# Kernel optimization log

Hardware: AMD Instinct MI355X
Metric: run time of the kernel (lower is better)

## Reference

```python
import jax, jax.numpy as jnp
import numpy as np

B, L, C = 4, 2048, 1024
NH, HD, INTER, K = 16, 64, 256, 16
LR = 1.0
EPS = 1e-6

def gelu_tanh(x):
    return 0.5 * x * (1.0 + jnp.tanh(0.79788456 * (x + 0.044715 * x * x * x)))

def diff_gelu(x):
    t = jnp.tanh(0.79788456 * x * (1.0 + 0.044715 * x * x))
    return 0.5 * x * ((1.0 - t * t) * (0.79788456 + 0.1070322243 * x * x)) + 0.5 * (1.0 + t)

def setup_inputs():
    key = jax.random.key(0)
    ks = jax.random.split(key, 8)
    num_layers = 24
    return {
        'hidden_states': jax.random.normal(ks[0], (B, L, C), jnp.float32),
        'Wq': 0.02 * jax.random.normal(ks[1], (C, C), jnp.float32),
        'Wk': 0.02 * jax.random.normal(ks[2], (C, C), jnp.float32),
        'Wv': 0.02 * jax.random.normal(ks[3], (C, C), jnp.float32),
        'Wo': 0.02 * jax.random.normal(ks[4], (C, C), jnp.float32),
        'W1': 0.02 * jax.random.normal(ks[5], (NH, HD, INTER), jnp.float32),
        'b1': jnp.zeros((NH, 1, INTER), jnp.float32),
        'W2': (0.02 / np.sqrt(2 * num_layers)) * jax.random.normal(ks[6], (NH, INTER, HD), jnp.float32),
        'b2': jnp.zeros((NH, 1, HD), jnp.float32),
        'ln_weight': jnp.ones((NH, HD), jnp.float32),
        'ln_bias': jnp.zeros((NH, HD), jnp.float32),
        'gate_weight': 0.02 * jax.random.normal(ks[7], (NH, 1, C), jnp.float32),
        'gate_bias': jnp.zeros((NH, 1), jnp.float32),
    }

def _ln(z, w, b):
    mu = z.mean(-1, keepdims=True)
    var = z.var(-1, keepdims=True)
    return w * ((z - mu) * jax.lax.rsqrt(var + EPS)) + b

def _compute_chunk(carry, inp, ln_w, ln_b):
    # One inner-SGD chunk (dual form), per batch/head.
    W1, b1, W2, b2 = carry                       # [HD,INTER],[1,INTER],[INTER,HD],[1,HD]
    XA, XB, XC, coeff = inp                      # [K,HD],[K,HD],[K,HD],[K,1]
    Z1 = XB @ W1 + b1                            # [K,INTER]
    X2 = gelu_tanh(Z1)
    Z2 = X2 @ W2 + b2                            # [K,HD]
    DLN_out, ln_vjp = jax.vjp(lambda z: _ln(z, ln_w, ln_b), Z2)
    grad_Z2 = ln_vjp(DLN_out - XA)[0]            # d(recon loss)/dZ2
    grad_Z1 = (grad_Z2 @ W2.T) * diff_gelu(Z1)
    Attn1 = jnp.tril(XC @ XB.T)                  # [K,K] causal dual-form attention
    b1_bar = b1 - coeff * jnp.cumsum(grad_Z1, axis=0)
    Z1_bar = XC @ W1 - (coeff * Attn1) @ grad_Z1 + b1_bar
    X2_bar = gelu_tanh(Z1_bar)
    Attn2 = jnp.tril(X2_bar @ X2.T)
    b2_bar = b2 - coeff * jnp.cumsum(grad_Z2, axis=0)
    Z2_bar = X2_bar @ W2 - (coeff * Attn2) @ grad_Z2 + b2_bar
    W1n = W1 - (coeff[-1] * XB).T @ grad_Z1
    W2n = W2 - (coeff[-1] * X2).T @ grad_Z2
    return (W1n, b1_bar[-1:], W2n, b2_bar[-1:]), Z2_bar

def _per_head(XA, XB, XC, coeff, W1, b1, W2, b2, ln_w, ln_b):
    step = lambda c, i: _compute_chunk(c, i, ln_w, ln_b)
    _, ys = jax.lax.scan(step, (W1, b1, W2, b2), (XA, XB, XC, coeff))
    return ys                                    # [n_chunk,K,HD]

def reference(hidden_states, Wq, Wk, Wv, Wo, W1, b1, W2, b2, ln_weight, ln_bias, gate_weight, gate_bias):
    n_chunk = L // K
    X = hidden_states.reshape(B, n_chunk, K, C)
    def proj(W):
        return (hidden_states @ W.T).reshape(B, n_chunk, K, NH, HD).transpose(0, 3, 1, 2, 4)
    XA, XB, XC = proj(Wq), proj(Wk), proj(Wv)    # [B,NH,n_chunk,K,HD]
    ilr = jax.nn.sigmoid(jnp.einsum('bnkc,hoc->bhnko', X, gate_weight) + gate_bias[None, :, None, None, :])
    token_idx = 1.0 / jnp.arange(1, K + 1, dtype=jnp.float32)
    coeff = (LR * token_idx).reshape(1, 1, 1, K, 1) * ilr / HD   # [B,NH,n_chunk,K,1]
    over_heads = jax.vmap(_per_head, in_axes=(0,) * 10)
    over_batch = jax.vmap(over_heads, in_axes=(0, 0, 0, 0) + (None,) * 6)
    ys = over_batch(XA, XB, XC, coeff, W1, b1, W2, b2, ln_weight, ln_bias)  # [B,NH,n_chunk,K,HD]
    XCW = ys.transpose(0, 2, 3, 1, 4).reshape(B, L, C)
    return XCW @ Wo.T
```

## Files before the change

### kernel.cpp

```cpp
#include <hip/hip_runtime.h>
#include <hip/hip_bf16.h>


#define B_  4
#define L_  2048
#define C_  1024
#define NH_ 16
#define HD_ 64
#define IN_ 256
#define K_  16
#define NCH_ 128
#define EPS_ 1e-6f

typedef unsigned short ushort_t;
typedef __attribute__((ext_vector_type(8))) short  s8v;
typedef __attribute__((ext_vector_type(4))) float  f4v;
typedef __attribute__((ext_vector_type(4))) unsigned short u4v;

#define MFMA(a,b,c) __builtin_amdgcn_mfma_f32_16x16x32_bf16(a,b,c,0,0,0)

#define LOAD_LDS16(gp, lp) \
  __builtin_amdgcn_global_load_lds((const __attribute__((address_space(1))) void*)(gp), \
                                   (__attribute__((address_space(3))) void*)(lp), 16, 0, 0)

__device__ __forceinline__ ushort_t f2bf(float f) {
    unsigned int u = __float_as_uint(f);
    unsigned int r = (u + 0x7FFFu + ((u >> 16) & 1u)) >> 16;
    return (ushort_t)r;
}
__device__ __forceinline__ float bf2f(ushort_t v) {
    return __uint_as_float(((unsigned int)v) << 16);
}
__device__ __forceinline__ float gelu_f(float x) {
    float u = 0.79788456f * (x + 0.044715f * x * x * x);
    return 0.5f * x * (1.0f + tanhf(u));
}
__device__ __forceinline__ float dgelu_f(float x) {
    float x2 = x * x;
    float t  = tanhf(0.79788456f * x * (1.0f + 0.044715f * x2));
    return 0.5f * x * ((1.0f - t * t) * (0.79788456f + 0.1070322243f * x2))
         + 0.5f * (1.0f + t);
}
__device__ __forceinline__ s8v ld4z(const ushort_t* p) {
    u4v v = *(const u4v*)p;
    s8v a = {(short)v[0], (short)v[1], (short)v[2], (short)v[3], 0, 0, 0, 0};
    return a;
}

__global__ void __launch_bounds__(256)
cast_kernel(const float* __restrict__ hid, const float* __restrict__ wq,
            const float* __restrict__ wk, const float* __restrict__ wv,
            const float* __restrict__ wo, ushort_t* __restrict__ dst)
{
    const long i = ((long)blockIdx.x * 256 + threadIdx.x) * 8;
    const float* src; long off;
    if (i < 8388608L)        { src = hid; off = i; }
    else if (i < 9437184L)   { src = wq;  off = i - 8388608L; }
    else if (i < 10485760L)  { src = wk;  off = i - 9437184L; }
    else if (i < 11534336L)  { src = wv;  off = i - 10485760L; }
    else                     { src = wo;  off = i - 11534336L; }
    float4 a = *(const float4*)(src + off);
    float4 b = *(const float4*)(src + off + 4);
    u4v p0, p1;
    p0[0] = f2bf(a.x); p0[1] = f2bf(a.y); p0[2] = f2bf(a.z); p0[3] = f2bf(a.w);
    p1[0] = f2bf(b.x); p1[1] = f2bf(b.y); p1[2] = f2bf(b.z); p1[3] = f2bf(b.w);
    *(u4v*)(dst + i)     = p0;
    *(u4v*)(dst + i + 4) = p1;
}

__global__ void __launch_bounds__(256, 2)
gemm_bf16(const ushort_t* __restrict__ A, const ushort_t* __restrict__ Bm,
          void* __restrict__ outp, int mode)
{
    __shared__ char lds[16384];
    char* Al = lds;
    char* Bl = lds + 8192;
    const int t  = threadIdx.x;
    const int w  = t >> 6, l = t & 63;
    const int lr = l & 15, lg = l >> 4;
    const int wm = w >> 1, wn = w & 1;
    const int wg = blockIdx.x;
    const int m0 = (wg >> 3) * 128, n0 = (wg & 7) * 128;

    f4v acc[4][4];
    #pragma unroll
    for (int i = 0; i < 4; ++i)
        #pragma unroll
        for (int j = 0; j < 4; ++j)
            acc[i][j] = (f4v){0.f, 0.f, 0.f, 0.f};

    const long arow0 = (long)(m0 + w * 16 + lr) * C_ + lg * 8;
    const long arow1 = (long)(m0 + (w + 4) * 16 + lr) * C_ + lg * 8;
    const long brow0 = (long)(n0 + w * 16 + lr) * C_ + lg * 8;
    const long brow1 = (long)(n0 + (w + 4) * 16 + lr) * C_ + lg * 8;

    for (int ks = 0; ks < C_ / 32; ++ks) {
        const int k0 = ks * 32;
        LOAD_LDS16(A  + arow0 + k0, Al + w * 1024);
        LOAD_LDS16(A  + arow1 + k0, Al + (w + 4) * 1024);
        LOAD_LDS16(Bm + brow0 + k0, Bl + w * 1024);
        LOAD_LDS16(Bm + brow1 + k0, Bl + (w + 4) * 1024);
        __syncthreads();
        s8v af[4], bfr[4];
        #pragma unroll
        for (int i = 0; i < 4; ++i)
            af[i] = *(const s8v*)(Al + (wm * 4 + i) * 1024 + l * 16);
        #pragma unroll
        for (int j = 0; j < 4; ++j)
            bfr[j] = *(const s8v*)(Bl + (wn * 4 + j) * 1024 + l * 16);
        #pragma unroll
        for (int i = 0; i < 4; ++i)
            #pragma unroll
            for (int j = 0; j < 4; ++j)
                acc[i][j] = MFMA(af[i], bfr[j], acc[i][j]);
        __syncthreads();
    }

    #pragma unroll
    for (int i = 0; i < 4; ++i) {
        #pragma unroll
        for (int j = 0; j < 4; ++j) {
            #pragma unroll
            for (int r = 0; r < 4; ++r) {
                const int grow = m0 + wm * 64 + i * 16 + lg * 4 + r;
                const int gcol = n0 + wn * 64 + j * 16 + lr;
                const float v = acc[i][j][r];
                if (mode == 2) {
                    ((float*)outp)[(long)grow * C_ + gcol] = v;
                } else {
                    const int bbv = grow >> 11, ll = grow & 2047;
                    const int hv = gcol >> 6, dv = gcol & 63;
                    const long addr = ((long)(bbv * NH_ + hv) * L_ + ll) * HD_ + dv;
                    if (mode == 0) ((float*)outp)[addr] = v;
                    else           ((ushort_t*)outp)[addr] = f2bf(v);
                }
            }
        }
    }
}

__global__ void __launch_bounds__(256)
gate_kernel(const float* __restrict__ X, const float* __restrict__ gw,
            const float* __restrict__ gb, float* __restrict__ coeff)
{
    __shared__ float Xs[16][132];
    __shared__ float Gs[16][132];
    const int t = threadIdx.x;
    const int row0 = blockIdx.x * 16;
    const int lsub = t >> 4, hh = t & 15;
    const int sr = t >> 4, sc0 = (t & 15) * 8;

    float accv = 0.f;
    for (int cb = 0; cb < C_; cb += 128) {
        float4 x0 = *(const float4*)&X [(long)(row0 + sr) * C_ + cb + sc0];
        float4 x1 = *(const float4*)&X [(long)(row0 + sr) * C_ + cb + sc0 + 4];
        float4 g0 = *(const float4*)&gw[(long)sr * C_ + cb + sc0];
        float4 g1 = *(const float4*)&gw[(long)sr * C_ + cb + sc0 + 4];
        *(float4*)&Xs[sr][sc0]     = x0; *(float4*)&Xs[sr][sc0 + 4] = x1;
        *(float4*)&Gs[sr][sc0]     = g0; *(float4*)&Gs[sr][sc0 + 4] = g1;
        __syncthreads();
        #pragma unroll 8
        for (int c = 0; c < 128; ++c) accv += Xs[lsub][c] * Gs[hh][c];
        __syncthreads();
    }
    const float ilr = 1.0f / (1.0f + __expf(-(accv + gb[hh])));
    const int l  = row0 + lsub;
    const int bb = l >> 11, lb = l & 2047;
    const int n  = lb >> 4, k = lb & 15;
    coeff[((long)(bb * NH_ + hh) * NCH_ + n) * K_ + k] =
        ilr / (64.0f * (float)(k + 1));
}

#define OFF_XBT    0
#define OFF_XCT    2304
#define OFF_XBT64  4608
#define OFF_W1T    7680
#define OFF_W2T    40448
#define OFF_W2BF   74240
#define OFF_X2     107008
#define OFF_X2T    115456
#define OFF_X2B    127744
#define OFF_GZ2    136192
#define OFF_GZ2T   138496
#define OFF_GZ1T   141568
#define OFF_M1     153856
#define OFF_M2     154624
#define OFF_Z2F    155392
#define OFF_B1S    159744
#define OFF_B2S    160768
#define OFF_LNW    161024
#define OFF_LNB    161280
#define OFF_CF     161536
#define SCAN_LDS_BYTES 161600

__global__ void __launch_bounds__(512, 1)
ttt_scan(const float* __restrict__ XAg, const ushort_t* __restrict__ XBg,
         const ushort_t* __restrict__ XCg, const float* __restrict__ coeff,
         const float* __restrict__ W1g, const float* __restrict__ b1g,
         const float* __restrict__ W2g, const float* __restrict__ b2g,
         const float* __restrict__ lnwg, const float* __restrict__ lnbg,
         ushort_t* __restrict__ XCWb)
{
    extern __shared__ char smb[];
    ushort_t* XBt_u   = (ushort_t*)(smb + OFF_XBT);
    ushort_t* XCt_u   = (ushort_t*)(smb + OFF_XCT);
    ushort_t* XBT64_u = (ushort_t*)(smb + OFF_XBT64);
    char*     W1Tb    = smb + OFF_W1T;
    ushort_t* W2T_u   = (ushort_t*)(smb + OFF_W2T);
    char*     W2bfb   = smb + OFF_W2BF;
    ushort_t* X2_u    = (ushort_t*)(smb + OFF_X2);
    ushort_t* X2T_u   = (ushort_t*)(smb + OFF_X2T);
    ushort_t* X2b_u   = (ushort_t*)(smb + OFF_X2B);
    ushort_t* gZ2_u   = (ushort_t*)(smb + OFF_GZ2);
    ushort_t* gZ2T_u  = (ushort_t*)(smb + OFF_GZ2T);
    ushort_t* gZ1T_u  = (ushort_t*)(smb + OFF_GZ1T);
    ushort_t* M1_u    = (ushort_t*)(smb + OFF_M1);
    ushort_t* M2_u    = (ushort_t*)(smb + OFF_M2);
    float* Z2f  = (float*)(smb + OFF_Z2F);
    float* b1s  = (float*)(smb + OFF_B1S);
    float* b2s  = (float*)(smb + OFF_B2S);
    float* lnws = (float*)(smb + OFF_LNW);
    float* lnbs = (float*)(smb + OFF_LNB);
    float* cf   = (float*)(smb + OFF_CF);

    const int t  = threadIdx.x;
    const int w  = t >> 6;
    const int l  = t & 63;
    const int lr = l & 15;
    const int lg = l >> 4;
    const int bh = blockIdx.x;
    const int h  = bh & 15;
    const int bb = bh >> 4;
    const long base = (long)bh * L_ * HD_;

    float w1r[32], w2r[32];
    #pragma unroll
    for (int i = 0; i < 8; ++i) {
        const int idx = 8 * w + i;
        const int mt = idx >> 4, nt = idx & 15;
        const int d0 = 16 * mt + 4 * lg, nn = 16 * nt + lr;
        #pragma unroll
        for (int r = 0; r < 4; ++r)
            w1r[4*i+r] = W1g[(h * HD_ + d0 + r) * IN_ + nn];
    }
    #pragma unroll
    for (int i = 0; i < 8; ++i) {
        const int idx = 8 * w + i;
        const int mt = idx >> 2, nt = idx & 3;
        const int j0 = 16 * mt + 4 * lg, dn = 16 * nt + lr;
        #pragma unroll
        for (int r = 0; r < 4; ++r)
            w2r[4*i+r] = W2g[(h * IN_ + j0 + r) * HD_ + dn];
    }
    #pragma unroll
    for (int i = 0; i < 8; ++i) {
        const int idx = 8 * w + i;
        const int mt = idx >> 4, nt = idx & 15;
        const int d0 = 16 * mt + 4 * lg, nn = 16 * nt + lr;
        u4v pw;
        #pragma unroll
        for (int r = 0; r < 4; ++r) pw[r] = f2bf(w1r[4*i+r]);
        *(u4v*)(W1Tb + nn * 128 + ((2 * d0) ^ ((nn & 7) << 4))) = pw;
    }
    #pragma unroll
    for (int i = 0; i < 8; ++i) {
        const int idx = 8 * w + i;
        const int mt = idx >> 2, nt = idx & 3;
        const int j0 = 16 * mt + 4 * lg, dn = 16 * nt + lr;
        u4v pw;
        #pragma unroll
        for (int r = 0; r < 4; ++r) pw[r] = f2bf(w2r[4*i+r]);
        *(u4v*)(W2T_u + dn * 264 + j0) = pw;
        #pragma unroll
        for (int r = 0; r < 4; ++r) {
            const int j = j0 + r;
            *(ushort_t*)(W2bfb + j * 128 + ((2 * dn) ^ ((j & 7) << 4))) = pw[r];
        }
    }
    if (t < 256) b1s[t] = b1g[h * IN_ + t];
    if (t < 64) {
        b2s[t]  = b2g[h * HD_ + t];
        lnws[t] = lnwg[h * HD_ + t];
        lnbs[t] = lnbg[h * HD_ + t];
    }
    __syncthreads();

    float z1f[8], z1b[8];
    f4v z2bacc;

    const int pkk = t >> 4, pd0 = (t & 15) * 4;
    u4v pf_b, pf_c; float4 pf_a; float pf_cf;
    if (t < 256) {
        pf_b = *(const u4v*)(XBg + base + (long)pkk * HD_ + pd0);
        pf_c = *(const u4v*)(XCg + base + (long)pkk * HD_ + pd0);
        pf_a = *(const float4*)&XAg[base + (long)pkk * HD_ + pd0];
    }
    if (t < 16) pf_cf = coeff[(long)bh * NCH_ * K_ + t];

    for (int n = 0; n < NCH_; ++n) {
        const int l0 = n << 4;
        float4 cur_a = pf_a;

        if (t < 256) {
            *(u4v*)(XBt_u + pkk * 72 + pd0) = pf_b;
            XBT64_u[(pd0+0) * 24 + pkk] = pf_b[0];
            XBT64_u[(pd0+1) * 24 + pkk] = pf_b[1];
            XBT64_u[(pd0+2) * 24 + pkk] = pf_b[2];
            XBT64_u[(pd0+3) * 24 + pkk] = pf_b[3];
            *(u4v*)(XCt_u + pkk * 72 + pd0) = pf_c;
        }
        if (t < 16) cf[t] = pf_cf;
        __syncthreads();
        const float c15 = cf[15];

        if (n + 1 < NCH_) {
            const long nb = base + (long)(l0 + 16 + pkk) * HD_ + pd0;
            if (t < 256) {
                pf_b = *(const u4v*)(XBg + nb);
                pf_c = *(const u4v*)(XCg + nb);
                pf_a = *(const float4*)&XAg[nb];
            }
            if (t < 16) pf_cf = coeff[((long)bh * NCH_ + n + 1) * K_ + t];
        }

        #pragma unroll
        for (int a = 0; a < 2; ++a) {
            const int n0 = 32 * w + 16 * a;
            const int nn = n0 + lr;
            const float bv = b1s[nn];
            f4v accZ = {bv, bv, bv, bv};
            f4v accB = accZ;
            #pragma unroll
            for (int ks = 0; ks < 2; ++ks) {
                s8v xb = *(const s8v*)(XBt_u + lr * 72 + 8 * lg + 32 * ks);
                s8v xc = *(const s8v*)(XCt_u + lr * 72 + 8 * lg + 32 * ks);
                s8v wf = *(const s8v*)(W1Tb + nn * 128 +
                                       ((16 * lg + 64 * ks) ^ ((nn & 7) << 4)));
                accZ = MFMA(xb, wf, accZ);
                accB = MFMA(xc, wf, accB);
            }
            u4v pkT;
            #pragma unroll
            for (int r = 0; r < 4; ++r) {
                z1f[4*a+r] = accZ[r];
                z1b[4*a+r] = accB[r];
                ushort_t bxx = f2bf(gelu_f(accZ[r]));
                X2_u[(4 * lg + r) * 264 + nn] = bxx;
                pkT[r] = bxx;
            }
            *(u4v*)(X2T_u + nn * 24 + 4 * lg) = pkT;
        }
        if (w == 0) {
            f4v at = {0.f, 0.f, 0.f, 0.f};
            #pragma unroll
            for (int ks = 0; ks < 2; ++ks) {
                s8v xc = *(const s8v*)(XCt_u + lr * 72 + 8 * lg + 32 * ks);
                s8v xb = *(const s8v*)(XBt_u + lr * 72 + 8 * lg + 32 * ks);
                at = MFMA(xc, xb, at);
            }
            #pragma unroll
            for (int r = 0; r < 4; ++r) {
                const int aa = 4 * lg + r;
                float val = (lr <= aa) ? -(cf[aa] * (at[r] + 1.0f)) : 0.0f;
                M1_u[aa * 24 + lr] = f2bf(val);
            }
        }
        __syncthreads();

        if (w < 4) {
            f4v acc = {0.f, 0.f, 0.f, 0.f};
            #pragma unroll
            for (int ks = 0; ks < 8; ++ks) {
                s8v xa = *(const s8v*)(X2_u + lr * 264 + 8 * lg + 32 * ks);
                s8v wt = *(const s8v*)(W2T_u + (16 * w + lr) * 264 + 8 * lg + 32 * ks);
                acc = MFMA(xa, wt, acc);
            }
            #pragma unroll
            for (int r = 0; r < 4; ++r)
                Z2f[(4 * lg + r) * 68 + 16 * w + lr] = acc[r];
        }
        __syncthreads();

        if (t < 256) {
            const int kk = t >> 4, d0 = pd0;
            float4 z = *(float4*)&Z2f[kk * 68 + d0];
            z.x += b2s[d0]; z.y += b2s[d0+1]; z.z += b2s[d0+2]; z.w += b2s[d0+3];
            float s = z.x + z.y + z.z + z.w;
            #pragma unroll
            for (int m = 1; m < 16; m <<= 1) s += __shfl_xor(s, m, 16);
            const float mu = s * (1.0f / 64.0f);
            const float e0 = z.x - mu, e1 = z.y - mu, e2 = z.z - mu, e3 = z.w - mu;
            float v = e0*e0 + e1*e1 + e2*e2 + e3*e3;
            #pragma unroll
            for (int m = 1; m < 16; m <<= 1) v += __shfl_xor(v, m, 16);
            const float rstd = rsqrtf(v * (1.0f / 64.0f) + EPS_);
            const float xh0 = e0*rstd, xh1 = e1*rstd, xh2 = e2*rstd, xh3 = e3*rstd;
            const float lw0 = lnws[d0+0], lw1 = lnws[d0+1], lw2 = lnws[d0+2], lw3 = lnws[d0+3];
            const float g0 = (lw0*xh0 + lnbs[d0+0]) - cur_a.x;
            const float g1 = (lw1*xh1 + lnbs[d0+1]) - cur_a.y;
            const float g2 = (lw2*xh2 + lnbs[d0+2]) - cur_a.z;
            const float g3 = (lw3*xh3 + lnbs[d0+3]) - cur_a.w;
            const float wg0 = lw0*g0, wg1 = lw1*g1, wg2 = lw2*g2, wg3 = lw3*g3;
            float sa  = wg0 + wg1 + wg2 + wg3;
            float sbv = wg0*xh0 + wg1*xh1 + wg2*xh2 + wg3*xh3;
            #pragma unroll
            for (int m = 1; m < 16; m <<= 1) {
                sa  += __shfl_xor(sa,  m, 16);
                sbv += __shfl_xor(sbv, m, 16);
            }
            const float mwg  = sa  * (1.0f / 64.0f);
            const float mwgx = sbv * (1.0f / 64.0f);
            u4v pg;
            pg[0] = f2bf(rstd * (wg0 - mwg - xh0 * mwgx));
            pg[1] = f2bf(rstd * (wg1 - mwg - xh1 * mwgx));
            pg[2] = f2bf(rstd * (wg2 - mwg - xh2 * mwgx));
            pg[3] = f2bf(rstd * (wg3 - mwg - xh3 * mwgx));
            *(u4v*)(gZ2_u + kk * 72 + d0) = pg;
            gZ2T_u[(d0+0) * 24 + kk] = pg[0];
            gZ2T_u[(d0+1) * 24 + kk] = pg[1];
            gZ2T_u[(d0+2) * 24 + kk] = pg[2];
            gZ2T_u[(d0+3) * 24 + kk] = pg[3];
        }
        __syncthreads();

        #pragma unroll
        for (int a = 0; a < 2; ++a) {
            const int n0 = 32 * w + 16 * a;
            const int nn = n0 + lr;
            f4v acc = {0.f, 0.f, 0.f, 0.f};
            #pragma unroll
            for (int ks = 0; ks < 2; ++ks) {
                s8v gz = *(const s8v*)(gZ2_u + lr * 72 + 8 * lg + 32 * ks);
                s8v wb = *(const s8v*)(W2bfb + nn * 128 +
                                       ((16 * lg + 64 * ks) ^ ((nn & 7) << 4)));
                acc = MFMA(gz, wb, acc);
            }
            u4v pk;
            #pragma unroll
            for (int r = 0; r < 4; ++r)
                pk[r] = f2bf(acc[r] * dgelu_f(z1f[4*a+r]));
            *(u4v*)(gZ1T_u + nn * 24 + 4 * lg) = pk;
        }
        __syncthreads();

        #pragma unroll
        for (int a = 0; a < 2; ++a) {
            const int nn = 32 * w + 16 * a + lr;
            s8v ml = ld4z(M1_u + lr * 24 + 4 * lg);
            s8v gr = ld4z(gZ1T_u + nn * 24 + 4 * lg);
            f4v acc = {z1b[4*a], z1b[4*a+1], z1b[4*a+2], z1b[4*a+3]};
            acc = MFMA(ml, gr, acc);
            #pragma unroll
            for (int r = 0; r < 4; ++r)
                X2b_u[(4 * lg + r) * 264 + nn] = f2bf(gelu_f(acc[r]));
        }
        #pragma unroll
        for (int i = 0; i < 8; ++i) {
            const int idx = 8 * w + i;
            const int mt = idx >> 4, nt = idx & 15;
            s8v la = ld4z(XBT64_u + (16 * mt + lr) * 24 + 4 * lg);
            s8v rb = ld4z(gZ1T_u + (16 * nt + lr) * 24 + 4 * lg);
            f4v uz = {0.f, 0.f, 0.f, 0.f};
            uz = MFMA(la, rb, uz);
            u4v pw;
            #pragma unroll
            for (int r = 0; r < 4; ++r) {
                w1r[4*i+r] -= c15 * uz[r];
                pw[r] = f2bf(w1r[4*i+r]);
            }
            const int nn1 = 16 * nt + lr;
            const int d0  = 16 * mt + 4 * lg;
            *(u4v*)(W1Tb + nn1 * 128 + ((2 * d0) ^ ((nn1 & 7) << 4))) = pw;
        }
        if (t < 256) {
            float s = 0.f;
            #pragma unroll
            for (int q = 0; q < 4; ++q) {
                u4v v = *(const u4v*)(gZ1T_u + t * 24 + 4 * q);
                s += bf2f(v[0]) + bf2f(v[1]) + bf2f(v[2]) + bf2f(v[3]);
            }
            b1s[t] -= c15 * s;
        }
        __syncthreads();

        if (w == 0) {
            f4v at2 = {0.f, 0.f, 0.f, 0.f};
            #pragma unroll
            for (int ks = 0; ks < 8; ++ks) {
                s8v xb2 = *(const s8v*)(X2b_u + lr * 264 + 8 * lg + 32 * ks);
                s8v x2r = *(const s8v*)(X2_u  + lr * 264 + 8 * lg + 32 * ks);
                at2 = MFMA(xb2, x2r, at2);
            }
            #pragma unroll
            for (int r = 0; r < 4; ++r) {
                const int aa = 4 * lg + r;
                float val = (lr <= aa) ? -(cf[aa] * (at2[r] + 1.0f)) : 0.0f;
                M2_u[aa * 24 + lr] = f2bf(val);
            }
        } else if (w <= 4) {
            const int dt = w - 1;
            const float bv = b2s[16 * dt + lr];
            z2bacc = (f4v){bv, bv, bv, bv};
            #pragma unroll
            for (int ks = 0; ks < 8; ++ks) {
                s8v xb2 = *(const s8v*)(X2b_u + lr * 264 + 8 * lg + 32 * ks);
                s8v wt  = *(const s8v*)(W2T_u + (16 * dt + lr) * 264 + 8 * lg + 32 * ks);
                z2bacc = MFMA(xb2, wt, z2bacc);
            }
        }
        #pragma unroll
        for (int i = 0; i < 8; ++i) {
            const int idx = 8 * w + i;
            const int mt = idx >> 2, nt = idx & 3;
            s8v la = ld4z(X2T_u  + (16 * mt + lr) * 24 + 4 * lg);
            s8v rb = ld4z(gZ2T_u + (16 * nt + lr) * 24 + 4 * lg);
            f4v uz = {0.f, 0.f, 0.f, 0.f};
            uz = MFMA(la, rb, uz);
            #pragma unroll
            for (int r = 0; r < 4; ++r) w2r[4*i+r] -= c15 * uz[r];
        }
        __syncthreads();

        if (w >= 1 && w <= 4) {
            const int dt = w - 1;
            s8v ml = ld4z(M2_u + lr * 24 + 4 * lg);
            s8v gr = ld4z(gZ2T_u + (16 * dt + lr) * 24 + 4 * lg);
            z2bacc = MFMA(ml, gr, z2bacc);
            #pragma unroll
            for (int r = 0; r < 4; ++r)
                XCWb[((long)(bb * L_ + l0 + 4 * lg + r)) * C_ + h * HD_ + 16 * dt + lr]
                    = f2bf(z2bacc[r]);
        }
        #pragma unroll
        for (int i = 0; i < 8; ++i) {
            const int idx = 8 * w + i;
            const int mt = idx >> 2, nt = idx & 3;
            const int j0 = 16 * mt + 4 * lg, dn = 16 * nt + lr;
            u4v pw;
            #pragma unroll
            for (int r = 0; r < 4; ++r) pw[r] = f2bf(w2r[4*i+r]);
            *(u4v*)(W2T_u + dn * 264 + j0) = pw;
            #pragma unroll
            for (int r = 0; r < 4; ++r) {
                const int j = j0 + r;
                *(ushort_t*)(W2bfb + j * 128 + ((2 * dn) ^ ((j & 7) << 4))) = pw[r];
            }
        }
        if (t < 64) {
            float s = 0.f;
            #pragma unroll
            for (int q = 0; q < 4; ++q) {
                u4v v = *(const u4v*)(gZ2T_u + t * 24 + 4 * q);
                s += bf2f(v[0]) + bf2f(v[1]) + bf2f(v[2]) + bf2f(v[3]);
            }
            b2s[t] -= c15 * s;
        }
        __syncthreads();
    }
}

extern "C" void kernel_launch(void* const* d_in, const int* in_sizes, int n_in,
                              void* d_out, int out_size, void* d_ws, size_t ws_size,
                              hipStream_t stream)
{
    const float* hidden = (const float*)d_in[0];
    const float* Wq  = (const float*)d_in[1];
    const float* Wk  = (const float*)d_in[2];
    const float* Wv  = (const float*)d_in[3];
    const float* Wo  = (const float*)d_in[4];
    const float* W1g = (const float*)d_in[5];
    const float* b1g = (const float*)d_in[6];
    const float* W2g = (const float*)d_in[7];
    const float* b2g = (const float*)d_in[8];
    const float* lnw = (const float*)d_in[9];
    const float* lnb = (const float*)d_in[10];
    const float* gw  = (const float*)d_in[11];
    const float* gb  = (const float*)d_in[12];
    float* out = (float*)d_out;
    char* ws  = (char*)d_ws;

    ushort_t* bfbuf  = (ushort_t*)(ws);
    ushort_t* hid_bf = bfbuf;
    ushort_t* Wq_bf  = bfbuf + 8388608L;
    ushort_t* Wk_bf  = Wq_bf + 1048576L;
    ushort_t* Wv_bf  = Wk_bf + 1048576L;
    ushort_t* Wo_bf  = Wv_bf + 1048576L;
    float*    XA     = (float*)(ws + 25165824L);
    ushort_t* XB_bf  = (ushort_t*)(ws + 58720256L);
    ushort_t* XC_bf  = (ushort_t*)(ws + 75497472L);
    ushort_t* XCW_bf = (ushort_t*)(ws + 92274688L);
    float*    coeff  = (float*)(ws + 109051904L);

    hipFuncSetAttribute(reinterpret_cast<const void*>(ttt_scan),
                        hipFuncAttributeMaxDynamicSharedMemorySize,
                        SCAN_LDS_BYTES);

    cast_kernel<<<6144, 256, 0, stream>>>(hidden, Wq, Wk, Wv, Wo, bfbuf);
    gemm_bf16<<<512, 256, 0, stream>>>(hid_bf, Wq_bf, XA,    0);
    gemm_bf16<<<512, 256, 0, stream>>>(hid_bf, Wk_bf, XB_bf, 1);
    gemm_bf16<<<512, 256, 0, stream>>>(hid_bf, Wv_bf, XC_bf, 1);
    gate_kernel<<<512, 256, 0, stream>>>(hidden, gw, gb, coeff);
    ttt_scan<<<64, 512, SCAN_LDS_BYTES, stream>>>(XA, XB_bf, XC_bf, coeff,
                                                  W1g, b1g, W2g, b2g,
                                                  lnw, lnb, XCW_bf);
    gemm_bf16<<<512, 256, 0, stream>>>(XCW_bf, Wo_bf, out, 2);
}
```

Measured before the change: 1.121 ms.

## Streamline TTT scan: fewer barriers, fast gelu, DPP reductions, padded LDS strides

Reworks the sequential TTT scan kernel in several ways. The mask computation and the Z2 GEMM now run in the same phase, and the grad-Z1 and X2-bar steps are fused, which removes several block-wide barriers per chunk. Tanh-based gelu and its derivative are replaced with exp plus reciprocal forms, cross-lane reductions use DPP instead of shuffles, and bf16 packing uses the native conversion. LDS transpose strides change from 24 to 28 to cut bank conflicts, and the two mask buffers are merged. The fast exp and reciprocal math changes numerics slightly, and the merged mask buffer relies on correct barrier placement.

```diff
diff --git a/kernel.cpp b/kernel.cpp
--- a/kernel.cpp
+++ b/kernel.cpp
@@ -16,6 +16,7 @@
 typedef __attribute__((ext_vector_type(8))) short  s8v;
 typedef __attribute__((ext_vector_type(4))) float  f4v;
 typedef __attribute__((ext_vector_type(4))) unsigned short u4v;
+typedef __attribute__((ext_vector_type(4))) __bf16 bf4v;
 
 #define MFMA(a,b,c) __builtin_amdgcn_mfma_f32_16x16x32_bf16(a,b,c,0,0,0)
 
@@ -24,27 +25,50 @@
                                    (__attribute__((address_space(3))) void*)(lp), 16, 0, 0)
 
 __device__ __forceinline__ ushort_t f2bf(float f) {
-    unsigned int u = __float_as_uint(f);
-    unsigned int r = (u + 0x7FFFu + ((u >> 16) & 1u)) >> 16;
-    return (ushort_t)r;
+    __bf16 h = (__bf16)f;
+    return __builtin_bit_cast(ushort_t, h);
+}
+__device__ __forceinline__ u4v pk4(float a, float b, float c, float d) {
+    bf4v h = {(__bf16)a, (__bf16)b, (__bf16)c, (__bf16)d};
+    return __builtin_bit_cast(u4v, h);
 }
 __device__ __forceinline__ float bf2f(ushort_t v) {
     return __uint_as_float(((unsigned int)v) << 16);
 }
-__device__ __forceinline__ float gelu_f(float x) {
+__device__ __forceinline__ float fast_gelu(float x) {
     float u = 0.79788456f * (x + 0.044715f * x * x * x);
-    return 0.5f * x * (1.0f + tanhf(u));
-}
-__device__ __forceinline__ float dgelu_f(float x) {
+    float e = __expf(2.0f * u);
+    float r = __builtin_amdgcn_rcpf(e + 1.0f);
+    return x - x * r;
+}
+__device__ __forceinline__ float fast_dgelu(float x) {
     float x2 = x * x;
-    float t  = tanhf(0.79788456f * x * (1.0f + 0.044715f * x2));
-    return 0.5f * x * ((1.0f - t * t) * (0.79788456f + 0.1070322243f * x2))
-         + 0.5f * (1.0f + t);
+    float u = 0.79788456f * x * (1.0f + 0.044715f * x2);
+    float e = fminf(__expf(2.0f * u), 1e30f);
+    float r = __builtin_amdgcn_rcpf(e + 1.0f);
+    return 2.0f * x * e * r * r * (0.79788456f + 0.1070322243f * x2) + 1.0f - r;
 }
 __device__ __forceinline__ s8v ld4z(const ushort_t* p) {
     u4v v = *(const u4v*)p;
     s8v a = {(short)v[0], (short)v[1], (short)v[2], (short)v[3], 0, 0, 0, 0};
     return a;
+}
+__device__ __forceinline__ s8v reg4z(u4v v) {
+    s8v a = {(short)v[0], (short)v[1], (short)v[2], (short)v[3], 0, 0, 0, 0};
+    return a;
+}
+template <int CTRL>
+__device__ __forceinline__ float dpp_add(float x) {
+    int t = __builtin_amdgcn_update_dpp(0, __builtin_bit_cast(int, x),
+                                        CTRL, 0xf, 0xf, true);
+    return x + __builtin_bit_cast(float, t);
+}
+__device__ __forceinline__ float row16_sum(float x) {
+    x = dpp_add<0xB1>(x);
+    x = dpp_add<0x4E>(x);
+    x = dpp_add<0x124>(x);
+    x = dpp_add<0x128>(x);
+    return x;
 }
 
 __global__ void __launch_bounds__(256)
@@ -61,11 +85,8 @@
     else                     { src = wo;  off = i - 11534336L; }
     float4 a = *(const float4*)(src + off);
     float4 b = *(const float4*)(src + off + 4);
-    u4v p0, p1;
-    p0[0] = f2bf(a.x); p0[1] = f2bf(a.y); p0[2] = f2bf(a.z); p0[3] = f2bf(a.w);
-    p1[0] = f2bf(b.x); p1[1] = f2bf(b.y); p1[2] = f2bf(b.z); p1[3] = f2bf(b.w);
-    *(u4v*)(dst + i)     = p0;
-    *(u4v*)(dst + i + 4) = p1;
+    *(u4v*)(dst + i)     = pk4(a.x, a.y, a.z, a.w);
+    *(u4v*)(dst + i + 4) = pk4(b.x, b.y, b.z, b.w);
 }
 
 __global__ void __launch_bounds__(256, 2)
@@ -174,24 +195,22 @@
 #define OFF_XBT    0
 #define OFF_XCT    2304
 #define OFF_XBT64  4608
-#define OFF_W1T    7680
-#define OFF_W2T    40448
-#define OFF_W2BF   74240
-#define OFF_X2     107008
-#define OFF_X2T    115456
-#define OFF_X2B    127744
-#define OFF_GZ2    136192
-#define OFF_GZ2T   138496
-#define OFF_GZ1T   141568
-#define OFF_M1     153856
-#define OFF_M2     154624
-#define OFF_Z2F    155392
-#define OFF_B1S    159744
-#define OFF_B2S    160768
-#define OFF_LNW    161024
-#define OFF_LNB    161280
-#define OFF_CF     161536
-#define SCAN_LDS_BYTES 161600
+#define OFF_W1T    8192
+#define OFF_W2T    40960
+#define OFF_W2BF   74752
+#define OFF_X2     107520
+#define OFF_X2T    115968
+#define OFF_X2B    130304
+#define OFF_GZ2    138752
+#define OFF_GZ2T   141056
+#define OFF_GZ1T   144640
+#define OFF_M      158976
+#define OFF_B1S    159872
+#define OFF_B2S    160896
+#define OFF_LNW    161152
+#define OFF_LNB    161408
+#define OFF_CF     161664
+#define SCAN_LDS_BYTES 161728
 
 __global__ void __launch_bounds__(512, 1)
 ttt_scan(const float* __restrict__ XAg, const ushort_t* __restrict__ XBg,
@@ -214,9 +233,8 @@
     ushort_t* gZ2_u   = (ushort_t*)(smb + OFF_GZ2);
     ushort_t* gZ2T_u  = (ushort_t*)(smb + OFF_GZ2T);
     ushort_t* gZ1T_u  = (ushort_t*)(smb + OFF_GZ1T);
-    ushort_t* M1_u    = (ushort_t*)(smb + OFF_M1);
-    ushort_t* M2_u    = (ushort_t*)(smb + OFF_M2);
-    float* Z2f  = (float*)(smb + OFF_Z2F);
+    ushort_t* M_u     = (ushort_t*)(smb + OFF_M);
+    float* Z2f  = (float*)(smb + OFF_X2B);
     float* b1s  = (float*)(smb + OFF_B1S);
     float* b2s  = (float*)(smb + OFF_B2S);
     float* lnws = (float*)(smb + OFF_LNW);
@@ -242,6 +260,8 @@
         #pragma unroll
         for (int r = 0; r < 4; ++r)
             w1r[4*i+r] = W1g[(h * HD_ + d0 + r) * IN_ + nn];
+        *(u4v*)(W1Tb + nn * 128 + ((2 * d0) ^ ((nn & 7) << 4))) =
+            pk4(w1r[4*i], w1r[4*i+1], w1r[4*i+2], w1r[4*i+3]);
     }
     #pragma unroll
     for (int i = 0; i < 8; ++i) {
@@ -251,25 +271,7 @@
         #pragma unroll
         for (int r = 0; r < 4; ++r)
             w2r[4*i+r] = W2g[(h * IN_ + j0 + r) * HD_ + dn];
-    }
-    #pragma unroll
-    for (int i = 0; i < 8; ++i) {
-        const int idx = 8 * w + i;
-        const int mt = idx >> 4, nt = idx & 15;
-        const int d0 = 16 * mt + 4 * lg, nn = 16 * nt + lr;
-        u4v pw;
-        #pragma unroll
-        for (int r = 0; r < 4; ++r) pw[r] = f2bf(w1r[4*i+r]);
-        *(u4v*)(W1Tb + nn * 128 + ((2 * d0) ^ ((nn & 7) << 4))) = pw;
-    }
-    #pragma unroll
-    for (int i = 0; i < 8; ++i) {
-        const int idx = 8 * w + i;
-        const int mt = idx >> 2, nt = idx & 3;
-        const int j0 = 16 * mt + 4 * lg, dn = 16 * nt + lr;
-        u4v pw;
-        #pragma unroll
-        for (int r = 0; r < 4; ++r) pw[r] = f2bf(w2r[4*i+r]);
+        u4v pw = pk4(w2r[4*i], w2r[4*i+1], w2r[4*i+2], w2r[4*i+3]);
         *(u4v*)(W2T_u + dn * 264 + j0) = pw;
         #pragma unroll
         for (int r = 0; r < 4; ++r) {
@@ -303,10 +305,10 @@
 
         if (t < 256) {
             *(u4v*)(XBt_u + pkk * 72 + pd0) = pf_b;
-            XBT64_u[(pd0+0) * 24 + pkk] = pf_b[0];
-            XBT64_u[(pd0+1) * 24 + pkk] = pf_b[1];
-            XBT64_u[(pd0+2) * 24 + pkk] = pf_b[2];
-            XBT64_u[(pd0+3) * 24 + pkk] = pf_b[3];
+            XBT64_u[(pd0+0) * 28 + pkk] = pf_b[0];
+            XBT64_u[(pd0+1) * 28 + pkk] = pf_b[1];
+            XBT64_u[(pd0+2) * 28 + pkk] = pf_b[2];
+            XBT64_u[(pd0+3) * 28 + pkk] = pf_b[3];
             *(u4v*)(XCt_u + pkk * 72 + pd0) = pf_c;
         }
         if (t < 16) cf[t] = pf_cf;
@@ -325,8 +327,7 @@
 
         #pragma unroll
         for (int a = 0; a < 2; ++a) {
-            const int n0 = 32 * w + 16 * a;
-            const int nn = n0 + lr;
+            const int nn = 32 * w + 16 * a + lr;
             const float bv = b1s[nn];
             f4v accZ = {bv, bv, bv, bv};
             f4v accB = accZ;
@@ -339,18 +340,33 @@
                 accZ = MFMA(xb, wf, accZ);
                 accB = MFMA(xc, wf, accB);
             }
-            u4v pkT;
+            float gl[4];
             #pragma unroll
             for (int r = 0; r < 4; ++r) {
                 z1f[4*a+r] = accZ[r];
                 z1b[4*a+r] = accB[r];
-                ushort_t bxx = f2bf(gelu_f(accZ[r]));
-                X2_u[(4 * lg + r) * 264 + nn] = bxx;
-                pkT[r] = bxx;
-            }
-            *(u4v*)(X2T_u + nn * 24 + 4 * lg) = pkT;
-        }
-        if (w == 0) {
+                gl[r] = fast_gelu(accZ[r]);
+            }
+            u4v pkT = pk4(gl[0], gl[1], gl[2], gl[3]);
+            #pragma unroll
+            for (int r = 0; r < 4; ++r)
+                X2_u[(4 * lg + r) * 264 + nn] = pkT[r];
+            *(u4v*)(X2T_u + nn * 28 + 4 * lg) = pkT;
+        }
+        __syncthreads();
+
+        if (w < 4) {
+            f4v acc = {0.f, 0.f, 0.f, 0.f};
+            #pragma unroll
+            for (int ks = 0; ks < 8; ++ks) {
+                s8v xa = *(const s8v*)(X2_u + lr * 264 + 8 * lg + 32 * ks);
+                s8v wt = *(const s8v*)(W2T_u + (16 * w + lr) * 264 + 8 * lg + 32 * ks);
+                acc = MFMA(xa, wt, acc);
+            }
+            #pragma unroll
+            for (int r = 0; r < 4; ++r)
+                Z2f[(4 * lg + r) * 68 + 16 * w + lr] = acc[r];
+        } else if (w == 4) {
             f4v at = {0.f, 0.f, 0.f, 0.f};
             #pragma unroll
             for (int ks = 0; ks < 2; ++ks) {
@@ -362,22 +378,8 @@
             for (int r = 0; r < 4; ++r) {
                 const int aa = 4 * lg + r;
                 float val = (lr <= aa) ? -(cf[aa] * (at[r] + 1.0f)) : 0.0f;
-                M1_u[aa * 24 + lr] = f2bf(val);
-            }
-        }
-        __syncthreads();
-
-        if (w < 4) {
-            f4v acc = {0.f, 0.f, 0.f, 0.f};
-            #pragma unroll
-            for (int ks = 0; ks < 8; ++ks) {
-                s8v xa = *(const s8v*)(X2_u + lr * 264 + 8 * lg + 32 * ks);
-                s8v wt = *(const s8v*)(W2T_u + (16 * w + lr) * 264 + 8 * lg + 32 * ks);
-                acc = MFMA(xa, wt, acc);
-            }
-            #pragma unroll
-            for (int r = 0; r < 4; ++r)
-                Z2f[(4 * lg + r) * 68 + 16 * w + lr] = acc[r];
+                M_u[aa * 28 + lr] = f2bf(val);
+            }
         }
         __syncthreads();
 
@@ -385,14 +387,9 @@
             const int kk = t >> 4, d0 = pd0;
             float4 z = *(float4*)&Z2f[kk * 68 + d0];
             z.x += b2s[d0]; z.y += b2s[d0+1]; z.z += b2s[d0+2]; z.w += b2s[d0+3];
-            float s = z.x + z.y + z.z + z.w;
-            #pragma unroll
-            for (int m = 1; m < 16; m <<= 1) s += __shfl_xor(s, m, 16);
-            const float mu = s * (1.0f / 64.0f);
+            const float mu = row16_sum(z.x + z.y + z.z + z.w) * (1.0f / 64.0f);
             const float e0 = z.x - mu, e1 = z.y - mu, e2 = z.z - mu, e3 = z.w - mu;
-            float v = e0*e0 + e1*e1 + e2*e2 + e3*e3;
-            #pragma unroll
-            for (int m = 1; m < 16; m <<= 1) v += __shfl_xor(v, m, 16);
+            const float v = row16_sum(e0*e0 + e1*e1 + e2*e2 + e3*e3);
             const float rstd = rsqrtf(v * (1.0f / 64.0f) + EPS_);
             const float xh0 = e0*rstd, xh1 = e1*rstd, xh2 = e2*rstd, xh3 = e3*rstd;
             const float lw0 = lnws[d0+0], lw1 = lnws[d0+1], lw2 = lnws[d0+2], lw3 = lnws[d0+3];
@@ -401,32 +398,24 @@
             const float g2 = (lw2*xh2 + lnbs[d0+2]) - cur_a.z;
             const float g3 = (lw3*xh3 + lnbs[d0+3]) - cur_a.w;
             const float wg0 = lw0*g0, wg1 = lw1*g1, wg2 = lw2*g2, wg3 = lw3*g3;
-            float sa  = wg0 + wg1 + wg2 + wg3;
-            float sbv = wg0*xh0 + wg1*xh1 + wg2*xh2 + wg3*xh3;
-            #pragma unroll
-            for (int m = 1; m < 16; m <<= 1) {
-                sa  += __shfl_xor(sa,  m, 16);
-                sbv += __shfl_xor(sbv, m, 16);
-            }
-            const float mwg  = sa  * (1.0f / 64.0f);
-            const float mwgx = sbv * (1.0f / 64.0f);
-            u4v pg;
-            pg[0] = f2bf(rstd * (wg0 - mwg - xh0 * mwgx));
-            pg[1] = f2bf(rstd * (wg1 - mwg - xh1 * mwgx));
-            pg[2] = f2bf(rstd * (wg2 - mwg - xh2 * mwgx));
-            pg[3] = f2bf(rstd * (wg3 - mwg - xh3 * mwgx));
+            const float mwg  = row16_sum(wg0 + wg1 + wg2 + wg3) * (1.0f / 64.0f);
+            const float mwgx = row16_sum(wg0*xh0 + wg1*xh1 + wg2*xh2 + wg3*xh3)
+                               * (1.0f / 64.0f);
+            u4v pg = pk4(rstd * (wg0 - mwg - xh0 * mwgx),
+                         rstd * (wg1 - mwg - xh1 * mwgx),
+                         rstd * (wg2 - mwg - xh2 * mwgx),
+                         rstd * (wg3 - mwg - xh3 * mwgx));
             *(u4v*)(gZ2_u + kk * 72 + d0) = pg;
-            gZ2T_u[(d0+0) * 24 + kk] = pg[0];
-            gZ2T_u[(d0+1) * 24 + kk] = pg[1];
-            gZ2T_u[(d0+2) * 24 + kk] = pg[2];
-            gZ2T_u[(d0+3) * 24 + kk] = pg[3];
+            gZ2T_u[(d0+0) * 28 + kk] = pg[0];
+            gZ2T_u[(d0+1) * 28 + kk] = pg[1];
+            gZ2T_u[(d0+2) * 28 + kk] = pg[2];
+            gZ2T_u[(d0+3) * 28 + kk] = pg[3];
         }
         __syncthreads();
 
         #pragma unroll
         for (int a = 0; a < 2; ++a) {
-            const int n0 = 32 * w + 16 * a;
-            const int nn = n0 + lr;
+            const int nn = 32 * w + 16 * a + lr;
             f4v acc = {0.f, 0.f, 0.f, 0.f};
             #pragma unroll
             for (int ks = 0; ks < 2; ++ks) {
@@ -435,54 +424,45 @@
                                        ((16 * lg + 64 * ks) ^ ((nn & 7) << 4)));
                 acc = MFMA(gz, wb, acc);
             }
-            u4v pk;
+            u4v pk = pk4(acc[0] * fast_dgelu(z1f[4*a+0]),
+                         acc[1] * fast_dgelu(z1f[4*a+1]),
+                         acc[2] * fast_dgelu(z1f[4*a+2]),
+                         acc[3] * fast_dgelu(z1f[4*a+3]));
+            *(u4v*)(gZ1T_u + nn * 28 + 4 * lg) = pk;
+            s8v ml = ld4z(M_u + lr * 28 + 4 * lg);
+            s8v gr = reg4z(pk);
+            f4v accB = {z1b[4*a], z1b[4*a+1], z1b[4*a+2], z1b[4*a+3]};
+            accB = MFMA(ml, gr, accB);
             #pragma unroll
             for (int r = 0; r < 4; ++r)
-                pk[r] = f2bf(acc[r] * dgelu_f(z1f[4*a+r]));
-            *(u4v*)(gZ1T_u + nn * 24 + 4 * lg) = pk;
-        }
-        __syncthreads();
-
-        #pragma unroll
-        for (int a = 0; a < 2; ++a) {
-            const int nn = 32 * w + 16 * a + lr;
-            s8v ml = ld4z(M1_u + lr * 24 + 4 * lg);
-            s8v gr = ld4z(gZ1T_u + nn * 24 + 4 * lg);
-            f4v acc = {z1b[4*a], z1b[4*a+1], z1b[4*a+2], z1b[4*a+3]};
-            acc = MFMA(ml, gr, acc);
-            #pragma unroll
-            for (int r = 0; r < 4; ++r)
-                X2b_u[(4 * lg + r) * 264 + nn] = f2bf(gelu_f(acc[r]));
-        }
+                X2b_u[(4 * lg + r) * 264 + nn] = f2bf(fast_gelu(accB[r]));
+        }
+        __syncthreads();
+
         #pragma unroll
         for (int i = 0; i < 8; ++i) {
             const int idx = 8 * w + i;
             const int mt = idx >> 4, nt = idx & 15;
-            s8v la = ld4z(XBT64_u + (16 * mt + lr) * 24 + 4 * lg);
-            s8v rb = ld4z(gZ1T_u + (16 * nt + lr) * 24 + 4 * lg);
+            s8v la = ld4z(XBT64_u + (16 * mt + lr) * 28 + 4 * lg);
+            s8v rb = ld4z(gZ1T_u + (16 * nt + lr) * 28 + 4 * lg);
             f4v uz = {0.f, 0.f, 0.f, 0.f};
             uz = MFMA(la, rb, uz);
-            u4v pw;
-            #pragma unroll
-            for (int r = 0; r < 4; ++r) {
-                w1r[4*i+r] -= c15 * uz[r];
-                pw[r] = f2bf(w1r[4*i+r]);
-            }
+            #pragma unroll
+            for (int r = 0; r < 4; ++r) w1r[4*i+r] -= c15 * uz[r];
             const int nn1 = 16 * nt + lr;
             const int d0  = 16 * mt + 4 * lg;
-            *(u4v*)(W1Tb + nn1 * 128 + ((2 * d0) ^ ((nn1 & 7) << 4))) = pw;
+            *(u4v*)(W1Tb + nn1 * 128 + ((2 * d0) ^ ((nn1 & 7) << 4))) =
+                pk4(w1r[4*i], w1r[4*i+1], w1r[4*i+2], w1r[4*i+3]);
         }
         if (t < 256) {
             float s = 0.f;
             #pragma unroll
             for (int q = 0; q < 4; ++q) {
-                u4v v = *(const u4v*)(gZ1T_u + t * 24 + 4 * q);
+                u4v v = *(const u4v*)(gZ1T_u + t * 28 + 4 * q);
                 s += bf2f(v[0]) + bf2f(v[1]) + bf2f(v[2]) + bf2f(v[3]);
             }
             b1s[t] -= c15 * s;
         }
-        __syncthreads();
-
         if (w == 0) {
             f4v at2 = {0.f, 0.f, 0.f, 0.f};
             #pragma unroll
@@ -495,7 +475,7 @@
             for (int r = 0; r < 4; ++r) {
                 const int aa = 4 * lg + r;
                 float val = (lr <= aa) ? -(cf[aa] * (at2[r] + 1.0f)) : 0.0f;
-                M2_u[aa * 24 + lr] = f2bf(val);
+                M_u[aa * 28 + lr] = f2bf(val);
             }
         } else if (w <= 4) {
             const int dt = w - 1;
@@ -512,8 +492,8 @@
         for (int i = 0; i < 8; ++i) {
             const int idx = 8 * w + i;
             const int mt = idx >> 2, nt = idx & 3;
-            s8v la = ld4z(X2T_u  + (16 * mt + lr) * 24 + 4 * lg);
-            s8v rb = ld4z(gZ2T_u + (16 * nt + lr) * 24 + 4 * lg);
+            s8v la = ld4z(X2T_u  + (16 * mt + lr) * 28 + 4 * lg);
+            s8v rb = ld4z(gZ2T_u + (16 * nt + lr) * 28 + 4 * lg);
             f4v uz = {0.f, 0.f, 0.f, 0.f};
             uz = MFMA(la, rb, uz);
             #pragma unroll
@@ -523,8 +503,8 @@
 
         if (w >= 1 && w <= 4) {
             const int dt = w - 1;
-            s8v ml = ld4z(M2_u + lr * 24 + 4 * lg);
-            s8v gr = ld4z(gZ2T_u + (16 * dt + lr) * 24 + 4 * lg);
+            s8v ml = ld4z(M_u + lr * 28 + 4 * lg);
+            s8v gr = ld4z(gZ2T_u + (16 * dt + lr) * 28 + 4 * lg);
             z2bacc = MFMA(ml, gr, z2bacc);
             #pragma unroll
             for (int r = 0; r < 4; ++r)
@@ -536,9 +516,7 @@
             const int idx = 8 * w + i;
             const int mt = idx >> 2, nt = idx & 3;
             const int j0 = 16 * mt + 4 * lg, dn = 16 * nt + lr;
-            u4v pw;
-            #pragma unroll
-            for (int r = 0; r < 4; ++r) pw[r] = f2bf(w2r[4*i+r]);
+            u4v pw = pk4(w2r[4*i], w2r[4*i+1], w2r[4*i+2], w2r[4*i+3]);
             *(u4v*)(W2T_u + dn * 264 + j0) = pw;
             #pragma unroll
             for (int r = 0; r < 4; ++r) {
@@ -550,7 +528,7 @@
             float s = 0.f;
             #pragma unroll
             for (int q = 0; q < 4; ++q) {
-                u4v v = *(const u4v*)(gZ2T_u + t * 24 + 4 * q);
+                u4v v = *(const u4v*)(gZ2T_u + t * 28 + 4 * q);
                 s += bf2f(v[0]) + bf2f(v[1]) + bf2f(v[2]) + bf2f(v[3]);
             }
             b2s[t] -= c15 * s;
@@ -591,9 +569,9 @@
     ushort_t* XCW_bf = (ushort_t*)(ws + 92274688L);
     float*    coeff  = (float*)(ws + 109051904L);
 
-    hipFuncSetAttribute(reinterpret_cast<const void*>(ttt_scan),
-                        hipFuncAttributeMaxDynamicSharedMemorySize,
-                        SCAN_LDS_BYTES);
+    (void)hipFuncSetAttribute(reinterpret_cast<const void*>(ttt_scan),
+                              hipFuncAttributeMaxDynamicSharedMemorySize,
+                              SCAN_LDS_BYTES);
 
     cast_kernel<<<6144, 256, 0, stream>>>(hidden, Wq, Wk, Wv, Wo, bfbuf);
     gemm_bf16<<<512, 256, 0, stream>>>(hid_bf, Wq_bf, XA,    0);
```

Result: faster. 914.4 us (-18.4%).
